# Performance work log

Measured on AMD Instinct MI355X. Metric: run time of the kernel, lower is better.

## Reference

```python
import jax, jax.numpy as jnp
import numpy as np

TAU = 0.5
EPS = 1e-8  # torch CosineSimilarity eps


def _normalize(v):
    # matches torch cosine sim: divide by max(||v||, eps)
    n = jnp.linalg.norm(v, axis=-1, keepdims=True)
    return v / jnp.maximum(n, EPS)


def setup_inputs() -> dict:
    key = jax.random.key(0)
    k1, k2 = jax.random.split(key)
    N, D = 4096, 256
    x = jax.random.normal(k1, (N, D), dtype=jnp.float32)
    y = jax.random.normal(k2, (N, D), dtype=jnp.float32)
    return {"x": x, "y": y}


def reference(x, y):
    n = x.shape[0]
    xn = _normalize(x)
    yn = _normalize(y)
    inv_tau = 1.0 / TAU
    sim_xx = (xn @ xn.T) * inv_tau  # [n, n]
    sim_yy = (yn @ yn.T) * inv_tau
    sim_xy = (xn @ yn.T) * inv_tau
    neg_inf = jnp.float32(-jnp.inf)
    diag = jnp.arange(n)
    sim_xx = sim_xx.at[diag, diag].set(neg_inf)
    sim_yy = sim_yy.at[diag, diag].set(neg_inf)
    scores1 = jnp.concatenate([sim_xy, sim_xx], axis=-1)          # [n, 2n]
    scores2 = jnp.concatenate([sim_yy, sim_xy.T], axis=-1)        # [n, 2n]
    scores = jnp.concatenate([scores1, scores2], axis=-2)          # [2n, 2n]
    targets = jnp.arange(2 * n)
    logp = jax.nn.log_softmax(scores, axis=-1)
    loss = -jnp.mean(logp[jnp.arange(2 * n), targets])
    return loss
```

## Files before the change

### kernel.cpp

```cpp
#include <hip/hip_runtime.h>
#include <hip/hip_bf16.h>


#define NROWS 8192
#define DDIM  256
#define BM    256
#define BN    32
#define COLSPLIT 16
#define COLS_PER (NROWS / COLSPLIT)
#define NT (COLS_PER / BN)

typedef __attribute__((ext_vector_type(8))) __bf16 bf16x8_t;
typedef __attribute__((ext_vector_type(4))) float  f32x4_t;

typedef __attribute__((address_space(1))) const void* as1_cvp;
typedef __attribute__((address_space(3))) void*       as3_vp;

#if __has_builtin(__builtin_amdgcn_exp2f)
#define EXP2F __builtin_amdgcn_exp2f
#else
#define EXP2F exp2f
#endif

#define TWO_LOG2E 2.8853900817779268f

__global__ __launch_bounds__(256) void normalize_diag_kernel(
    const float* __restrict__ x, const float* __restrict__ y,
    __hip_bfloat16* __restrict__ zb, float* __restrict__ rowdiag,
    float* __restrict__ rowsum) {
  const int g = blockIdx.x * 256 + threadIdx.x;
  if (g < NROWS) rowsum[g] = 0.f;

  const int w = threadIdx.x >> 6, lane = threadIdx.x & 63;
  const int i = blockIdx.x * 4 + w;
  const float4 xv = ((const float4*)(x + (size_t)i * DDIM))[lane];
  const float4 yv = ((const float4*)(y + (size_t)i * DDIM))[lane];
  float ssx = xv.x * xv.x + xv.y * xv.y + xv.z * xv.z + xv.w * xv.w;
  float ssy = yv.x * yv.x + yv.y * yv.y + yv.z * yv.z + yv.w * yv.w;
  float sxy = xv.x * yv.x + xv.y * yv.y + xv.z * yv.z + xv.w * yv.w;
  #pragma unroll
  for (int off = 32; off > 0; off >>= 1) {
    ssx += __shfl_xor(ssx, off, 64);
    ssy += __shfl_xor(ssy, off, 64);
    sxy += __shfl_xor(sxy, off, 64);
  }
  const float sclx = 1.0f / fmaxf(sqrtf(ssx), 1e-8f);
  const float scly = 1.0f / fmaxf(sqrtf(ssy), 1e-8f);
  __hip_bfloat16 px[4], py[4];
  px[0] = __float2bfloat16(xv.x * sclx); px[1] = __float2bfloat16(xv.y * sclx);
  px[2] = __float2bfloat16(xv.z * sclx); px[3] = __float2bfloat16(xv.w * sclx);
  py[0] = __float2bfloat16(yv.x * scly); py[1] = __float2bfloat16(yv.y * scly);
  py[2] = __float2bfloat16(yv.z * scly); py[3] = __float2bfloat16(yv.w * scly);
  *(short4*)(zb + (size_t)i * DDIM + lane * 4)            = *(short4*)px;
  *(short4*)(zb + (size_t)(i + 4096) * DDIM + lane * 4)   = *(short4*)py;
  if (lane == 0) rowdiag[i] = 2.0f * sxy * sclx * scly;
}

__global__ __launch_bounds__(512) void gram_lse_kernel(
    const __hip_bfloat16* __restrict__ zbh, float* __restrict__ rowsum) {
  __shared__ short smem[4][BN * DDIM];

  const short* zs = (const short*)zbh;
  const char* zbytes = (const char*)zs;
  const int tid  = threadIdx.x;
  const int w    = tid >> 6;
  const int lane = tid & 63;
  const int lhi  = lane >> 4;
  const int llo  = lane & 15;
  const int i0 = (blockIdx.x >> 4) * BM;
  const int c0 = (blockIdx.x & 15) * COLS_PER;
  const bool has_diag = ((blockIdx.x >> 5) == (blockIdx.x & 15));

  const int arow0 = i0 + w * 32 + llo;
  const float TBF = __bfloat162float(__float2bfloat16(TWO_LOG2E));
  bf16x8_t afa[8], afb[8];
  #pragma unroll
  for (int ks = 0; ks < 8; ++ks) {
    afa[ks] = *(const bf16x8_t*)(zs + (size_t)arow0 * DDIM + ks * 32 + lhi * 8);
    afb[ks] = *(const bf16x8_t*)(zs + (size_t)(arow0 + 16) * DDIM + ks * 32 + lhi * 8);
    #pragma unroll
    for (int e = 0; e < 8; ++e) {
      afa[ks][e] = (__bf16)((float)afa[ks][e] * TBF);
      afb[ks][e] = (__bf16)((float)afb[ks][e] * TBF);
    }
  }

  int soff[2], loff[2];
  #pragma unroll
  for (int it = 0; it < 2; ++it) {
    const int o    = it * 8192 + tid * 16;
    const int cr   = o >> 9;
    const int slot = (o >> 4) & 31;
    soff[it] = cr * 512 + ((slot ^ cr) << 4);
    loff[it] = it * 8192 + w * 1024;
  }

#define STAGE1(buf_, ct_, it_) do {                                           \
    const size_t cbase_ = (size_t)(c0 + (ct_) * BN) * 512;                    \
    __builtin_amdgcn_global_load_lds(                                         \
        (as1_cvp)(zbytes + cbase_ + (size_t)soff[it_]),                       \
        (as3_vp)((char*)smem[buf_] + loff[it_]), 16, 0, 0);                   \
  } while (0)

  float racc0[4] = {0.f, 0.f, 0.f, 0.f};
  float racc1[4] = {0.f, 0.f, 0.f, 0.f};
  const int gr0 = i0 + w * 32 + lhi * 4;
  const int gr1 = gr0 + 16;

  #pragma unroll
  for (int t = 0; t < 3; ++t) {
    STAGE1(t, t, 0);
    STAGE1(t, t, 1);
  }

#define TILE(ct_, VMSTR) do {                                                 \
    asm volatile("s_waitcnt " VMSTR ::: "memory");                            \
    __syncthreads();                                                          \
    const int cb = c0 + (ct_) * BN;                                           \
    const short* bufp = smem[(ct_) & 3];                                      \
    _Pragma("unroll")                                                         \
    for (int nt = 0; nt < 2; ++nt) {                                          \
      if ((ct_) + 3 < NT) STAGE1(((ct_) + 3) & 3, (ct_) + 3, nt);             \
      const int cr = nt * 16 + llo;                                           \
      f32x4_t acc0 = {0.f, 0.f, 0.f, 0.f};                                    \
      f32x4_t acc1 = {0.f, 0.f, 0.f, 0.f};                                    \
      __builtin_amdgcn_s_setprio(1);                                          \
      _Pragma("unroll")                                                       \
      for (int ks = 0; ks < 8; ++ks) {                                        \
        const int kg = ks * 4 + lhi;                                          \
        const bf16x8_t bfrag = *(const bf16x8_t*)(                            \
            (const char*)bufp + cr * 512 + ((kg ^ cr) << 4));                 \
        acc0 = __builtin_amdgcn_mfma_f32_16x16x32_bf16(afa[ks], bfrag, acc0, 0, 0, 0); \
        acc1 = __builtin_amdgcn_mfma_f32_16x16x32_bf16(afb[ks], bfrag, acc1, 0, 0, 0); \
      }                                                                       \
      __builtin_amdgcn_s_setprio(0);                                          \
      if (has_diag) {                                                         \
        const int gc = cb + cr;                                               \
        _Pragma("unroll")                                                     \
        for (int j = 0; j < 4; ++j) {                                         \
          racc0[j] += ((gr0 + j) != gc) ? EXP2F(acc0[j]) : 0.f;               \
          racc1[j] += ((gr1 + j) != gc) ? EXP2F(acc1[j]) : 0.f;               \
        }                                                                     \
      } else {                                                                \
        _Pragma("unroll")                                                     \
        for (int j = 0; j < 4; ++j) {                                         \
          racc0[j] += EXP2F(acc0[j]);                                         \
          racc1[j] += EXP2F(acc1[j]);                                         \
        }                                                                     \
      }                                                                       \
    }                                                                         \
  } while (0)

  for (int ct = 0; ct < NT - 2; ++ct) TILE(ct, "vmcnt(4)");
  TILE(NT - 2, "vmcnt(2)");
  TILE(NT - 1, "vmcnt(0)");
#undef TILE
#undef STAGE1

  #pragma unroll
  for (int j = 0; j < 4; ++j) {
    float v0 = racc0[j], v1 = racc1[j];
    v0 += __shfl_xor(v0, 1, 16); v1 += __shfl_xor(v1, 1, 16);
    v0 += __shfl_xor(v0, 2, 16); v1 += __shfl_xor(v1, 2, 16);
    v0 += __shfl_xor(v0, 4, 16); v1 += __shfl_xor(v1, 4, 16);
    v0 += __shfl_xor(v0, 8, 16); v1 += __shfl_xor(v1, 8, 16);
    if (llo == 0) {
      atomicAdd(&rowsum[gr0 + j], v0);
      atomicAdd(&rowsum[gr1 + j], v1);
    }
  }
}

__global__ __launch_bounds__(256) void finalize_kernel(
    const float* __restrict__ rowsum, const float* __restrict__ rowdiag,
    float* __restrict__ out) {
  const int t = threadIdx.x;
  float s = 0.f;
  for (int r4 = t; r4 < NROWS / 4; r4 += 256) {
    const float4 v = ((const float4*)rowsum)[r4];
    s += __logf(v.x) + __logf(v.y) + __logf(v.z) + __logf(v.w);
  }
  for (int i4 = t; i4 < 4096 / 4; i4 += 256) {
    const float4 d = ((const float4*)rowdiag)[i4];
    s -= 2.0f * (d.x + d.y + d.z + d.w);
  }
  #pragma unroll
  for (int off = 32; off > 0; off >>= 1) s += __shfl_xor(s, off, 64);
  __shared__ float wsum[4];
  const int w = t >> 6, lane = t & 63;
  if (lane == 0) wsum[w] = s;
  __syncthreads();
  if (t == 0) out[0] = (wsum[0] + wsum[1] + wsum[2] + wsum[3]) / (float)NROWS;
}

extern "C" void kernel_launch(void* const* d_in, const int* in_sizes, int n_in,
                              void* d_out, int out_size, void* d_ws, size_t ws_size,
                              hipStream_t stream) {
  const float* x = (const float*)d_in[0];
  const float* y = (const float*)d_in[1];
  float* out = (float*)d_out;

  char* ws = (char*)d_ws;
  __hip_bfloat16* zb = (__hip_bfloat16*)ws;
  float* rowsum  = (float*)(ws + (size_t)NROWS * DDIM * 2);
  float* rowdiag = rowsum + NROWS;

  normalize_diag_kernel<<<1024, 256, 0, stream>>>(x, y, zb, rowdiag, rowsum);
  gram_lse_kernel<<<512, 512, 0, stream>>>(zb, rowsum);
  finalize_kernel<<<1, 256, 0, stream>>>(rowsum, rowdiag, out);
}
```

Baseline: 56.73 us.

## Software-pipeline LDS B-fragment loads with MFMA and raise occupancy hint

Restructures the per-tile inner loop into an explicit double-buffered register schedule. LDS reads for the next pair of k-steps are issued while MFMAs run on the previous pair, and the exp epilogue of the first column subtile is interleaved with the second subtile's loads. Both async global-to-LDS prefetches are hoisted to the top of the tile. It also adds a min-blocks hint of 4 to launch bounds, which caps registers per thread and risks spills given the 16 A-fragment registers held per thread.

```diff
diff --git a/kernel.cpp b/kernel.cpp
--- a/kernel.cpp
+++ b/kernel.cpp
@@ -56,7 +56,7 @@
   if (lane == 0) rowdiag[i] = 2.0f * sxy * sclx * scly;
 }
 
-__global__ __launch_bounds__(512) void gram_lse_kernel(
+__global__ __launch_bounds__(512, 4) void gram_lse_kernel(
     const __hip_bfloat16* __restrict__ zbh, float* __restrict__ rowsum) {
   __shared__ short smem[4][BN * DDIM];
 
@@ -104,69 +104,94 @@
 
   float racc0[4] = {0.f, 0.f, 0.f, 0.f};
   float racc1[4] = {0.f, 0.f, 0.f, 0.f};
+  f32x4_t acc0 = {0.f, 0.f, 0.f, 0.f};
+  f32x4_t acc1 = {0.f, 0.f, 0.f, 0.f};
   const int gr0 = i0 + w * 32 + lhi * 4;
   const int gr1 = gr0 + 16;
 
-  #pragma unroll
-  for (int t = 0; t < 3; ++t) {
-    STAGE1(t, t, 0);
-    STAGE1(t, t, 1);
-  }
+  bf16x8_t u0, u1, v0, v1;
+
+#define LDB2(D0, D1, ntv, kk) do {                                            \
+    const int cr_ = (ntv) * 16 + llo;                                         \
+    const char* rp_ = (const char*)bufp + cr_ * 512;                          \
+    D0 = *(const bf16x8_t*)(rp_ + (((((kk)    ) * 4 + lhi) ^ cr_) << 4));     \
+    D1 = *(const bf16x8_t*)(rp_ + (((((kk) + 1) * 4 + lhi) ^ cr_) << 4));     \
+  } while (0)
+
+#define CL2(S0, S1, kk) do {                                                  \
+    __builtin_amdgcn_s_setprio(1);                                            \
+    acc0 = __builtin_amdgcn_mfma_f32_16x16x32_bf16(afa[kk],     S0, acc0, 0, 0, 0); \
+    acc1 = __builtin_amdgcn_mfma_f32_16x16x32_bf16(afb[kk],     S0, acc1, 0, 0, 0); \
+    acc0 = __builtin_amdgcn_mfma_f32_16x16x32_bf16(afa[kk + 1], S1, acc0, 0, 0, 0); \
+    acc1 = __builtin_amdgcn_mfma_f32_16x16x32_bf16(afb[kk + 1], S1, acc1, 0, 0, 0); \
+    __builtin_amdgcn_s_setprio(0);                                            \
+  } while (0)
+
+#define EPI(ntv) do {                                                         \
+    const int gc_ = cb + (ntv) * 16 + llo;                                    \
+    if (has_diag) {                                                           \
+      _Pragma("unroll")                                                       \
+      for (int j = 0; j < 4; ++j) {                                           \
+        racc0[j] += ((gr0 + j) != gc_) ? EXP2F(acc0[j]) : 0.f;                \
+        racc1[j] += ((gr1 + j) != gc_) ? EXP2F(acc1[j]) : 0.f;                \
+      }                                                                       \
+    } else {                                                                  \
+      _Pragma("unroll")                                                       \
+      for (int j = 0; j < 4; ++j) {                                           \
+        racc0[j] += EXP2F(acc0[j]);                                           \
+        racc1[j] += EXP2F(acc1[j]);                                           \
+      }                                                                       \
+    }                                                                         \
+    acc0 = (f32x4_t){0.f, 0.f, 0.f, 0.f};                                     \
+    acc1 = (f32x4_t){0.f, 0.f, 0.f, 0.f};                                     \
+  } while (0)
 
 #define TILE(ct_, VMSTR) do {                                                 \
     asm volatile("s_waitcnt " VMSTR ::: "memory");                            \
     __syncthreads();                                                          \
     const int cb = c0 + (ct_) * BN;                                           \
     const short* bufp = smem[(ct_) & 3];                                      \
-    _Pragma("unroll")                                                         \
-    for (int nt = 0; nt < 2; ++nt) {                                          \
-      if ((ct_) + 3 < NT) STAGE1(((ct_) + 3) & 3, (ct_) + 3, nt);             \
-      const int cr = nt * 16 + llo;                                           \
-      f32x4_t acc0 = {0.f, 0.f, 0.f, 0.f};                                    \
-      f32x4_t acc1 = {0.f, 0.f, 0.f, 0.f};                                    \
-      __builtin_amdgcn_s_setprio(1);                                          \
-      _Pragma("unroll")                                                       \
-      for (int ks = 0; ks < 8; ++ks) {                                        \
-        const int kg = ks * 4 + lhi;                                          \
-        const bf16x8_t bfrag = *(const bf16x8_t*)(                            \
-            (const char*)bufp + cr * 512 + ((kg ^ cr) << 4));                 \
-        acc0 = __builtin_amdgcn_mfma_f32_16x16x32_bf16(afa[ks], bfrag, acc0, 0, 0, 0); \
-        acc1 = __builtin_amdgcn_mfma_f32_16x16x32_bf16(afb[ks], bfrag, acc1, 0, 0, 0); \
-      }                                                                       \
-      __builtin_amdgcn_s_setprio(0);                                          \
-      if (has_diag) {                                                         \
-        const int gc = cb + cr;                                               \
-        _Pragma("unroll")                                                     \
-        for (int j = 0; j < 4; ++j) {                                         \
-          racc0[j] += ((gr0 + j) != gc) ? EXP2F(acc0[j]) : 0.f;               \
-          racc1[j] += ((gr1 + j) != gc) ? EXP2F(acc1[j]) : 0.f;               \
-        }                                                                     \
-      } else {                                                                \
-        _Pragma("unroll")                                                     \
-        for (int j = 0; j < 4; ++j) {                                         \
-          racc0[j] += EXP2F(acc0[j]);                                         \
-          racc1[j] += EXP2F(acc1[j]);                                         \
-        }                                                                     \
-      }                                                                       \
+    if ((ct_) + 3 < NT) {                                                     \
+      STAGE1(((ct_) + 3) & 3, (ct_) + 3, 0);                                  \
+      STAGE1(((ct_) + 3) & 3, (ct_) + 3, 1);                                  \
     }                                                                         \
-  } while (0)
+    LDB2(u0, u1, 0, 0);                                                       \
+    LDB2(v0, v1, 0, 2);  CL2(u0, u1, 0);                                      \
+    LDB2(u0, u1, 0, 4);  CL2(v0, v1, 2);                                      \
+    LDB2(v0, v1, 0, 6);  CL2(u0, u1, 4);                                      \
+    LDB2(u0, u1, 1, 0);  CL2(v0, v1, 6);                                      \
+    LDB2(v0, v1, 1, 2);  EPI(0);  CL2(u0, u1, 0);                             \
+    LDB2(u0, u1, 1, 4);  CL2(v0, v1, 2);                                      \
+    LDB2(v0, v1, 1, 6);  CL2(u0, u1, 4);                                      \
+    CL2(v0, v1, 6);                                                           \
+    EPI(1);                                                                   \
+  } while (0)
+
+  #pragma unroll
+  for (int t = 0; t < 3; ++t) {
+    STAGE1(t, t, 0);
+    STAGE1(t, t, 1);
+  }
 
   for (int ct = 0; ct < NT - 2; ++ct) TILE(ct, "vmcnt(4)");
   TILE(NT - 2, "vmcnt(2)");
   TILE(NT - 1, "vmcnt(0)");
 #undef TILE
+#undef EPI
+#undef CL2
+#undef LDB2
 #undef STAGE1
 
   #pragma unroll
   for (int j = 0; j < 4; ++j) {
-    float v0 = racc0[j], v1 = racc1[j];
-    v0 += __shfl_xor(v0, 1, 16); v1 += __shfl_xor(v1, 1, 16);
-    v0 += __shfl_xor(v0, 2, 16); v1 += __shfl_xor(v1, 2, 16);
-    v0 += __shfl_xor(v0, 4, 16); v1 += __shfl_xor(v1, 4, 16);
-    v0 += __shfl_xor(v0, 8, 16); v1 += __shfl_xor(v1, 8, 16);
+    float p0 = racc0[j], p1 = racc1[j];
+    p0 += __shfl_xor(p0, 1, 16); p1 += __shfl_xor(p1, 1, 16);
+    p0 += __shfl_xor(p0, 2, 16); p1 += __shfl_xor(p1, 2, 16);
+    p0 += __shfl_xor(p0, 4, 16); p1 += __shfl_xor(p1, 4, 16);
+    p0 += __shfl_xor(p0, 8, 16); p1 += __shfl_xor(p1, 8, 16);
     if (llo == 0) {
-      atomicAdd(&rowsum[gr0 + j], v0);
-      atomicAdd(&rowsum[gr1 + j], v1);
+      atomicAdd(&rowsum[gr0 + j], p0);
+      atomicAdd(&rowsum[gr1 + j], p1);
     }
   }
 }
```

New measurement: 81.24 us. +43.2%, slower.
